# Kernel tuning notes

Hardware: AMD Instinct MI355X
Metric: run time of the kernel (lower is better)

## Reference

```python
import jax, jax.numpy as jnp
import numpy as np

N_NODES = 100000
HID = 128
N_LAYERS = 3
N_EDGES = 1600000
EPS = 1e-5


def setup_inputs() -> dict:
    key = jax.random.key(0)
    ks = jax.random.split(key, 10)
    H, L = HID, N_LAYERS
    # edge_index: row 0 = src, row 1 = dst (PyG source_to_target flow)
    edge_index = jax.random.randint(ks[0], (2, N_EDGES), 0, N_NODES, dtype=jnp.int32)
    # xavier-uniform embedding
    lim = float(np.sqrt(6.0 / (N_NODES + H)))
    emb = jax.random.uniform(ks[1], (N_NODES, H), jnp.float32, -lim, lim)
    s = 1.0 / np.sqrt(H)
    Wl = jax.random.uniform(ks[2], (L, H, H), jnp.float32, -s, s)  # lin_l (neighbors), has bias
    bl = jax.random.uniform(ks[3], (L, H), jnp.float32, -s, s)
    Wr = jax.random.uniform(ks[4], (L, H, H), jnp.float32, -s, s)  # lin_r (root), no bias
    ln_gamma = jnp.ones((L, H), jnp.float32)
    ln_beta = jnp.zeros((L, H), jnp.float32)
    sj = 1.0 / np.sqrt(H * (L + 1))
    jkW = jax.random.uniform(ks[5], (H, H * (L + 1)), jnp.float32, -sj, sj)
    jkb = jax.random.uniform(ks[6], (H,), jnp.float32, -sj, sj)
    return {"emb": emb, "Wl": Wl, "bl": bl, "Wr": Wr,
            "ln_gamma": ln_gamma, "ln_beta": ln_beta,
            "jkW": jkW, "jkb": jkb, "edge_index": edge_index}


def _layernorm(x, gamma, beta):
    mu = jnp.mean(x, axis=-1, keepdims=True)
    var = jnp.mean(jnp.square(x - mu), axis=-1, keepdims=True)
    return (x - mu) * jax.lax.rsqrt(var + EPS) * gamma + beta


def reference(emb, Wl, bl, Wr, ln_gamma, ln_beta, jkW, jkb, edge_index):
    src, dst = edge_index[0], edge_index[1]
    n = emb.shape[0]
    # in-degree for mean aggregation (clamped to avoid div-by-zero)
    deg = jax.ops.segment_sum(jnp.ones_like(dst, dtype=emb.dtype), dst, num_segments=n)
    inv_deg = (1.0 / jnp.maximum(deg, 1.0))[:, None]
    x = emb
    xs = [x]
    for i in range(N_LAYERS):
        x_prev = x
        # scatter-mean of neighbor features (gather [E,H] -> segment_sum [N,H])
        agg = jax.ops.segment_sum(x[src], dst, num_segments=n) * inv_deg
        # SAGEConv: lin_l(agg) + lin_r(x)
        x = agg @ Wl[i].T + bl[i] + x @ Wr[i].T
        x = _layernorm(x, ln_gamma[i], ln_beta[i])
        x = jax.nn.relu(x)
        # dropout is identity in eval mode
        if i > 0:
            x = x + x_prev
        xs.append(x)
    # jumping-knowledge concat + projection
    x = jnp.concatenate(xs, axis=1) @ jkW.T + jkb
    return x
```

## Files before the change

### kernel.cpp

```cpp
#include <hip/hip_runtime.h>
#include <hip/hip_bf16.h>
#include <stdint.h>

#define HID 128
#define BSHIFT 7
#define NBLK 64

typedef __attribute__((ext_vector_type(8))) __bf16 bf16x8;
typedef __attribute__((ext_vector_type(4))) float f32x4;

static __device__ __forceinline__ float bf2f(ushort h){
  union { uint u; float f; } c; c.u = ((uint)h) << 16; return c.f;
}
static __device__ __forceinline__ ushort f2bf(float f){
  union { float f; uint u; } c; c.f = f;
  uint u = c.u;
  return (ushort)((u + 0x7fffu + ((u >> 16) & 1u)) >> 16);
}
static __device__ __forceinline__ bf16x8 load8(const ushort* p){
  return *(const bf16x8*)p;
}

__global__ void k_cvt(const float* __restrict__ in, ushort* __restrict__ out, int n){
  int i = blockIdx.x * 256 + threadIdx.x;
  if (i < n) out[i] = f2bf(in[i]);
}

__global__ void k_cvtw(const float* __restrict__ Wl, const float* __restrict__ Wr,
                       ushort* __restrict__ outF, int total){
  int o = blockIdx.x * 256 + threadIdx.x;
  if (o >= total) return;
  int layer = o >> 15;
  int r = o & 32767;
  int e    = r & 7;
  int lane = (r >> 3) & 63;
  int jt   = (r >> 9) & 7;
  int mat  = (r >> 12) & 1;
  int kt   = r >> 13;
  int l16 = lane & 15, quad = lane >> 4;
  int j = l16 * 8 + jt;
  int k = kt * 32 + quad * 8 + e;
  const float* W = mat ? Wr : Wl;
  outF[o] = f2bf(W[layer * 16384 + j * 128 + k]);
}

__global__ void k_cvtjk(const float* __restrict__ jkW, ushort* __restrict__ outF){
  int o = blockIdx.x * 256 + threadIdx.x;
  int e    = o & 7;
  int lane = (o >> 3) & 63;
  int jt   = (o >> 9) & 7;
  int kt   = o >> 12;
  int l16 = lane & 15, quad = lane >> 4;
  int j = l16 * 4 + (jt & 3) + (jt >> 2) * 64;
  int k = kt * 32 + quad * 8 + e;
  outF[o] = f2bf(jkW[j * 512 + k]);
}

__global__ __launch_bounds__(1024) void k_count(
    const int* __restrict__ dst, int* __restrict__ rowcnt, int E, int NB, int es){
  __shared__ int h[1024];
  int blk = blockIdx.x;
  for (int i = threadIdx.x; i < NB; i += 1024) h[i] = 0;
  __syncthreads();
  int e0 = blk * es, e1 = min(e0 + es, E);
  for (int e = e0 + threadIdx.x; e < e1; e += 1024)
    atomicAdd(&h[dst[e] >> BSHIFT], 1);
  __syncthreads();
  for (int i = threadIdx.x; i < NB; i += 1024)
    rowcnt[blk * NB + i] = h[i];
}

__global__ __launch_bounds__(1024) void k_colscan(
    int* __restrict__ rowcnt, int* __restrict__ bbase, int NB, int nblk){
  int b = threadIdx.x;
  int total = 0;
  if (b < NB)
    for (int r = 0; r < nblk; r++) total += rowcnt[r * NB + b];
  int lane = b & 63, w = b >> 6;
  int x = total;
  #pragma unroll
  for (int d = 1; d < 64; d <<= 1){ int y = __shfl_up(x, d, 64); if (lane >= d) x += y; }
  __shared__ int tmp[16];
  if (lane == 63) tmp[w] = x;
  __syncthreads();
  if (b < 64){
    int s = (lane < 16) ? tmp[lane] : 0;
    #pragma unroll
    for (int d = 1; d < 16; d <<= 1){ int y = __shfl_up(s, d, 64); if (lane >= d) s += y; }
    if (lane < 16) tmp[lane] = s;
  }
  __syncthreads();
  int base = ((w > 0) ? tmp[w - 1] : 0) + x - total;
  if (b < NB){
    bbase[b] = base;
    int acc = base;
    for (int r = 0; r < nblk; r++){
      int v = rowcnt[r * NB + b];
      rowcnt[r * NB + b] = acc;
      acc += v;
    }
    if (b == NB - 1) bbase[NB] = acc;
  }
}

__global__ __launch_bounds__(1024) void k_place(
    const int* __restrict__ src, const int* __restrict__ dst,
    const int* __restrict__ rowcnt, uint* __restrict__ binned, int E, int NB, int es){
  __shared__ int cur[1024];
  int blk = blockIdx.x;
  for (int i = threadIdx.x; i < NB; i += 1024) cur[i] = rowcnt[blk * NB + i];
  __syncthreads();
  int e0 = blk * es, e1 = min(e0 + es, E);
  for (int e = e0 + threadIdx.x; e < e1; e += 1024){
    int d = dst[e];
    int b = d >> BSHIFT;
    int pos = atomicAdd(&cur[b], 1);
    binned[pos] = ((uint)src[e] << BSHIFT) | (uint)(d & 127);
  }
}

__global__ __launch_bounds__(256) void k_bpass(
    const uint* __restrict__ binned, const int* __restrict__ bbase,
    int* __restrict__ csr, int* __restrict__ offs, int* __restrict__ cnt, int N){
  int b = blockIdx.x;
  int n0 = b << BSHIFT;
  int tid = threadIdx.x;
  __shared__ int lcnt[128], loffs[128];
  if (tid < 128) lcnt[tid] = 0;
  __syncthreads();
  int base = bbase[b];
  int m = bbase[b + 1] - base;
  const uint* bp = binned + base;
  uint vv[12]; int slot[12];
  #pragma unroll
  for (int u = 0; u < 12; u++){
    int i = tid + u * 256;
    if (i < m){
      uint v = bp[i];
      vv[u] = v;
      slot[u] = atomicAdd(&lcnt[v & 127], 1);
    }
  }
  __syncthreads();
  if (tid < 64){
    int a0 = lcnt[tid * 2], a1 = lcnt[tid * 2 + 1];
    int s = a0 + a1;
    int x = s;
    #pragma unroll
    for (int d = 1; d < 64; d <<= 1){ int y = __shfl_up(x, d, 64); if (tid >= d) x += y; }
    int excl = x - s;
    loffs[tid * 2] = excl;
    loffs[tid * 2 + 1] = excl + a0;
  }
  __syncthreads();
  if (tid < 128 && n0 + tid < N){
    cnt[n0 + tid] = lcnt[tid];
    offs[n0 + tid] = base + loffs[tid];
  }
  #pragma unroll
  for (int u = 0; u < 12; u++){
    int i = tid + u * 256;
    if (i < m){
      uint v = vv[u];
      csr[base + loffs[v & 127] + slot[u]] = (int)(v >> BSHIFT);
    }
  }
}

__global__ __launch_bounds__(256) void k_aggregate(
    const ushort* __restrict__ x, const int* __restrict__ csr,
    const int* __restrict__ offs, const int* __restrict__ cnt,
    ushort* __restrict__ agg, int N){
  int node = blockIdx.x * 4 + (threadIdx.x >> 6);
  int lane = threadIdx.x & 63;
  if (node >= N) return;
  int half = lane >> 5;
  int l32  = lane & 31;
  int beg = offs[node], d = cnt[node];
  if (d == 0){
    if (half == 0){
      uint2 z = {0u, 0u};
      *(uint2*)(agg + (size_t)node * HID + l32 * 4) = z;
    }
    return;
  }
  const int* __restrict__ cp = csr + beg;
  float s0 = 0.f, s1 = 0.f, s2 = 0.f, s3 = 0.f;
  int i = 0;
  for (; i + 16 <= d; i += 16){
    int idx[8];
    #pragma unroll
    for (int u = 0; u < 8; u++) idx[u] = cp[i + 2 * u + half];
    uint2 v[8];
    #pragma unroll
    for (int u = 0; u < 8; u++)
      v[u] = *(const uint2*)(x + (size_t)idx[u] * HID + l32 * 4);
    #pragma unroll
    for (int u = 0; u < 8; u++){
      s0 += bf2f((ushort)v[u].x);
      s1 += bf2f((ushort)(v[u].x >> 16));
      s2 += bf2f((ushort)v[u].y);
      s3 += bf2f((ushort)(v[u].y >> 16));
    }
  }
  if (i < d){
    int idx[8]; float w[8];
    #pragma unroll
    for (int u = 0; u < 8; u++){
      int pos = i + 2 * u + half;
      bool ok = pos < d;
      pos = ok ? pos : d - 1;
      idx[u] = cp[pos];
      w[u] = ok ? 1.f : 0.f;
    }
    uint2 v[8];
    #pragma unroll
    for (int u = 0; u < 8; u++)
      v[u] = *(const uint2*)(x + (size_t)idx[u] * HID + l32 * 4);
    #pragma unroll
    for (int u = 0; u < 8; u++){
      s0 = fmaf(w[u], bf2f((ushort)v[u].x), s0);
      s1 = fmaf(w[u], bf2f((ushort)(v[u].x >> 16)), s1);
      s2 = fmaf(w[u], bf2f((ushort)v[u].y), s2);
      s3 = fmaf(w[u], bf2f((ushort)(v[u].y >> 16)), s3);
    }
  }
  s0 += __shfl_xor(s0, 32, 64);
  s1 += __shfl_xor(s1, 32, 64);
  s2 += __shfl_xor(s2, 32, 64);
  s3 += __shfl_xor(s3, 32, 64);
  if (half == 0){
    float inv = 1.0f / fmaxf((float)d, 1.0f);
    uint2 o;
    o.x = (uint)f2bf(s0 * inv) | ((uint)f2bf(s1 * inv) << 16);
    o.y = (uint)f2bf(s2 * inv) | ((uint)f2bf(s3 * inv) << 16);
    *(uint2*)(agg + (size_t)node * HID + l32 * 4) = o;
  }
}

template<int HAS_RES>
__global__ __launch_bounds__(256, 2) void k_layer(
    const ushort* __restrict__ agg, const ushort* __restrict__ xin,
    const ushort* __restrict__ Wf,
    const float* __restrict__ bl, const float* __restrict__ gamma,
    const float* __restrict__ beta,
    ushort* __restrict__ xout, int N, int nTiles){
  __shared__ ushort sB[32768];
  int tid = threadIdx.x;
  int wv = tid >> 6, lane = tid & 63;
  int quad = lane >> 4, l16 = lane & 15;

  #pragma unroll
  for (int i = 0; i < 16; i++){
    int c = i * 256 + tid;
    *(bf16x8*)(sB + c * 8) = load8(Wf + c * 8);
  }
  __syncthreads();

  float4 bi0 = *(const float4*)(bl + l16 * 8);
  float4 bi1 = *(const float4*)(bl + l16 * 8 + 4);
  float4 g0 = *(const float4*)(gamma + l16 * 8);
  float4 g1 = *(const float4*)(gamma + l16 * 8 + 4);
  float4 be0 = *(const float4*)(beta + l16 * 8);
  float4 be1 = *(const float4*)(beta + l16 * 8 + 4);
  float gg[8] = {g0.x, g0.y, g0.z, g0.w, g1.x, g1.y, g1.z, g1.w};
  float bb[8] = {be0.x, be0.y, be0.z, be0.w, be1.x, be1.y, be1.z, be1.w};
  float bia[8] = {bi0.x, bi0.y, bi0.z, bi0.w, bi1.x, bi1.y, bi1.z, bi1.w};

  for (int tile = blockIdx.x; tile < nTiles; tile += gridDim.x){
    int rowbase = tile * 128 + wv * 32;
    int r0 = rowbase + l16;      if (r0 >= N) r0 = N - 1;
    int r1 = rowbase + 16 + l16; if (r1 >= N) r1 = N - 1;

    bf16x8 aL0[4], aL1[4], aR0[4], aR1[4];
    #pragma unroll
    for (int kt = 0; kt < 4; kt++){
      int ao = kt * 32 + quad * 8;
      aL0[kt] = load8(agg + (size_t)r0 * HID + ao);
      aL1[kt] = load8(agg + (size_t)r1 * HID + ao);
      aR0[kt] = load8(xin + (size_t)r0 * HID + ao);
      aR1[kt] = load8(xin + (size_t)r1 * HID + ao);
    }

    f32x4 acc[2][8];
    #pragma unroll
    for (int jt = 0; jt < 8; jt++){
      float b = bia[jt];
      f32x4 c = {b, b, b, b};
      acc[0][jt] = c; acc[1][jt] = c;
    }

    #pragma unroll
    for (int kt = 0; kt < 4; kt++){
      #pragma unroll
      for (int jt = 0; jt < 8; jt++){
        bf16x8 bL = load8(sB + ((kt * 16 + jt) * 64 + lane) * 8);
        bf16x8 bR = load8(sB + ((kt * 16 + 8 + jt) * 64 + lane) * 8);
        acc[0][jt] = __builtin_amdgcn_mfma_f32_16x16x32_bf16(aL0[kt], bL, acc[0][jt], 0, 0, 0);
        acc[1][jt] = __builtin_amdgcn_mfma_f32_16x16x32_bf16(aL1[kt], bL, acc[1][jt], 0, 0, 0);
        acc[0][jt] = __builtin_amdgcn_mfma_f32_16x16x32_bf16(aR0[kt], bR, acc[0][jt], 0, 0, 0);
        acc[1][jt] = __builtin_amdgcn_mfma_f32_16x16x32_bf16(aR1[kt], bR, acc[1][jt], 0, 0, 0);
      }
    }

    #pragma unroll
    for (int rt = 0; rt < 2; rt++){
      float s1[4] = {0,0,0,0}, s2[4] = {0,0,0,0};
      #pragma unroll
      for (int jt = 0; jt < 8; jt++){
        #pragma unroll
        for (int r = 0; r < 4; r++){ float v = acc[rt][jt][r]; s1[r] += v; s2[r] += v * v; }
      }
      #pragma unroll
      for (int m = 1; m < 16; m <<= 1){
        #pragma unroll
        for (int r = 0; r < 4; r++){
          s1[r] += __shfl_xor(s1[r], m, 64);
          s2[r] += __shfl_xor(s2[r], m, 64);
        }
      }
      #pragma unroll
      for (int r = 0; r < 4; r++){
        float mu = s1[r] * (1.f / 128.f);
        float var = s2[r] * (1.f / 128.f) - mu * mu;
        float rs = rsqrtf(var + 1e-5f);
        int row = rowbase + rt * 16 + quad * 4 + r;
        int rowc = row < N ? row : N - 1;
        uint rw[4] = {0u, 0u, 0u, 0u};
        if (HAS_RES){
          uint4 rv = *(const uint4*)(xin + (size_t)rowc * HID + l16 * 8);
          rw[0] = rv.x; rw[1] = rv.y; rw[2] = rv.z; rw[3] = rv.w;
        }
        uint ow[4];
        #pragma unroll
        for (int p = 0; p < 4; p++){
          float v0 = (acc[rt][2 * p][r] - mu) * rs * gg[2 * p] + bb[2 * p];
          float v1 = (acc[rt][2 * p + 1][r] - mu) * rs * gg[2 * p + 1] + bb[2 * p + 1];
          v0 = fmaxf(v0, 0.f);
          v1 = fmaxf(v1, 0.f);
          if (HAS_RES){
            v0 += bf2f((ushort)(rw[p] & 0xffffu));
            v1 += bf2f((ushort)(rw[p] >> 16));
          }
          ow[p] = (uint)f2bf(v0) | ((uint)f2bf(v1) << 16);
        }
        uint4 o;
        o.x = ow[0]; o.y = ow[1]; o.z = ow[2]; o.w = ow[3];
        if (row < N)
          *(uint4*)(xout + (size_t)row * HID + l16 * 8) = o;
      }
    }
  }
}

__global__ __launch_bounds__(256, 2) void k_jk(
    const ushort* __restrict__ emb, const ushort* __restrict__ x1,
    const ushort* __restrict__ x2, const ushort* __restrict__ x3,
    const ushort* __restrict__ Wf,
    const float* __restrict__ jkb, float* __restrict__ out, int N, int nTiles){
  __shared__ ushort sB[32768];
  int tid = threadIdx.x;
  int wv = tid >> 6, lane = tid & 63;
  int quad = lane >> 4, l16 = lane & 15;

  float4 jb0 = *(const float4*)(jkb + l16 * 4);
  float4 jb1 = *(const float4*)(jkb + 64 + l16 * 4);
  float bia[8] = {jb0.x, jb0.y, jb0.z, jb0.w, jb1.x, jb1.y, jb1.z, jb1.w};

  for (int tile = blockIdx.x; tile < nTiles; tile += gridDim.x){
    int rowbase = tile * 128 + wv * 32;
    int r0 = rowbase + l16;      if (r0 >= N) r0 = N - 1;
    int r1 = rowbase + 16 + l16; if (r1 >= N) r1 = N - 1;

    f32x4 acc[2][8];
    #pragma unroll
    for (int jt = 0; jt < 8; jt++){
      float b = bia[jt];
      f32x4 c = {b, b, b, b};
      acc[0][jt] = c; acc[1][jt] = c;
    }

    #pragma unroll
    for (int h = 0; h < 2; h++){
      const ushort* sA = h ? x2 : emb;
      const ushort* sC = h ? x3 : x1;
      bf16x8 aA0[4], aA1[4], aC0[4], aC1[4];
      #pragma unroll
      for (int kt = 0; kt < 4; kt++){
        int ao = kt * 32 + quad * 8;
        aA0[kt] = load8(sA + (size_t)r0 * HID + ao);
        aA1[kt] = load8(sA + (size_t)r1 * HID + ao);
        aC0[kt] = load8(sC + (size_t)r0 * HID + ao);
        aC1[kt] = load8(sC + (size_t)r1 * HID + ao);
      }
      __syncthreads();
      const ushort* src = Wf + h * 32768;
      #pragma unroll
      for (int i = 0; i < 16; i++){
        int c = i * 256 + tid;
        *(bf16x8*)(sB + c * 8) = load8(src + c * 8);
      }
      __syncthreads();
      #pragma unroll
      for (int kt = 0; kt < 4; kt++){
        #pragma unroll
        for (int jt = 0; jt < 8; jt++){
          bf16x8 bA = load8(sB + ((kt * 8 + jt) * 64 + lane) * 8);
          bf16x8 bC = load8(sB + (((4 + kt) * 8 + jt) * 64 + lane) * 8);
          acc[0][jt] = __builtin_amdgcn_mfma_f32_16x16x32_bf16(aA0[kt], bA, acc[0][jt], 0, 0, 0);
          acc[1][jt] = __builtin_amdgcn_mfma_f32_16x16x32_bf16(aA1[kt], bA, acc[1][jt], 0, 0, 0);
          acc[0][jt] = __builtin_amdgcn_mfma_f32_16x16x32_bf16(aC0[kt], bC, acc[0][jt], 0, 0, 0);
          acc[1][jt] = __builtin_amdgcn_mfma_f32_16x16x32_bf16(aC1[kt], bC, acc[1][jt], 0, 0, 0);
        }
      }
    }

    #pragma unroll
    for (int rt = 0; rt < 2; rt++){
      #pragma unroll
      for (int r = 0; r < 4; r++){
        int row = rowbase + rt * 16 + quad * 4 + r;
        if (row < N){
          f32x4 v0 = {acc[rt][0][r], acc[rt][1][r], acc[rt][2][r], acc[rt][3][r]};
          f32x4 v1 = {acc[rt][4][r], acc[rt][5][r], acc[rt][6][r], acc[rt][7][r]};
          *(f32x4*)(out + (size_t)row * HID + l16 * 4) = v0;
          *(f32x4*)(out + (size_t)row * HID + 64 + l16 * 4) = v1;
        }
      }
    }
  }
}

extern "C" void kernel_launch(void* const* d_in, const int* in_sizes, int n_in,
                              void* d_out, int out_size, void* d_ws, size_t ws_size,
                              hipStream_t stream){
  const float* emb   = (const float*)d_in[0];
  const float* Wl    = (const float*)d_in[1];
  const float* bl    = (const float*)d_in[2];
  const float* Wr    = (const float*)d_in[3];
  const float* gamma = (const float*)d_in[4];
  const float* beta  = (const float*)d_in[5];
  const float* jkW   = (const float*)d_in[6];
  const float* jkb   = (const float*)d_in[7];
  const int*   eidx  = (const int*)d_in[8];
  int N = in_sizes[0] / HID;
  int E = in_sizes[8] / 2;
  const int* src = eidx;
  const int* dst = eidx + E;
  float* out = (float*)d_out;

  int NB = (N + 127) >> BSHIFT;
  int es = (E + NBLK - 1) / NBLK;

  char* w = (char*)d_ws;
  auto carve = [&](size_t bytes) -> char* {
    char* p = w; w += (bytes + 255) & ~(size_t)255; return p;
  };
  int Npad = ((N + 127) / 128) * 128;
  int* rowcnt   = (int*)carve((size_t)NBLK * NB * 4);
  int* bbase    = (int*)carve((size_t)(NB + 1) * 4);
  uint* binned  = (uint*)carve((size_t)E * 4);
  int* cnt      = (int*)carve((size_t)N * 4);
  int* offs     = (int*)carve((size_t)N * 4);
  int* csr      = (int*)carve((size_t)E * 4);
  ushort* Wfrag = (ushort*)carve((size_t)3 * 32768 * 2);
  ushort* jkWf  = (ushort*)carve((size_t)65536 * 2);
  ushort* embbf = (ushort*)carve((size_t)Npad * HID * 2);
  ushort* agg   = (ushort*)carve((size_t)Npad * HID * 2);
  ushort* x1    = (ushort*)carve((size_t)Npad * HID * 2);
  ushort* x2    = (ushort*)carve((size_t)Npad * HID * 2);
  ushort* x3    = (ushort*)carve((size_t)Npad * HID * 2);

  int nEmb = N * HID;
  k_cvtw<<<(3 * 32768 + 255) / 256, 256, 0, stream>>>(Wl, Wr, Wfrag, 3 * 32768);
  k_cvtjk<<<65536 / 256, 256, 0, stream>>>(jkW, jkWf);
  k_cvt<<<(nEmb + 255) / 256, 256, 0, stream>>>(emb, embbf, nEmb);

  k_count<<<NBLK, 1024, 0, stream>>>(dst, rowcnt, E, NB, es);
  k_colscan<<<1, 1024, 0, stream>>>(rowcnt, bbase, NB, NBLK);
  k_place<<<NBLK, 1024, 0, stream>>>(src, dst, rowcnt, binned, E, NB, es);
  k_bpass<<<NB, 256, 0, stream>>>(binned, bbase, csr, offs, cnt, N);

  int aggBlocks = (N + 3) / 4;
  int nTiles = (N + 127) / 128;
  int gemmGrid = nTiles < 512 ? nTiles : 512;

  k_aggregate<<<aggBlocks, 256, 0, stream>>>(embbf, csr, offs, cnt, agg, N);
  k_layer<0><<<gemmGrid, 256, 0, stream>>>(agg, embbf, Wfrag, bl, gamma, beta, x1, N, nTiles);
  k_aggregate<<<aggBlocks, 256, 0, stream>>>(x1, csr, offs, cnt, agg, N);
  k_layer<1><<<gemmGrid, 256, 0, stream>>>(agg, x1, Wfrag + 32768, bl + HID,
                                           gamma + HID, beta + HID, x2, N, nTiles);
  k_aggregate<<<aggBlocks, 256, 0, stream>>>(x2, csr, offs, cnt, agg, N);
  k_layer<1><<<gemmGrid, 256, 0, stream>>>(agg, x2, Wfrag + 2 * 32768, bl + 2 * HID,
                                           gamma + 2 * HID, beta + 2 * HID, x3, N, nTiles);
  k_jk<<<gemmGrid, 256, 0, stream>>>(embbf, x1, x2, x3, jkWf, jkb, out, N, nTiles);
}
```

Before: 631.4 us.

## Keep full JK weight resident in LDS and use 512-thread blocks in k_jk

The JK projection kernel now loads the whole bf16 jkW fragment (128 KB) into LDS once per block, instead of reloading two halves into LDS on every tile with two barriers each. Blocks become 512 threads covering 256-row tiles, and the grid is capped at 256. This removes the per-tile weight reload traffic and synchronisation. The cost is that 128 KB of LDS per block limits how many blocks fit on a CU, so occupancy is likely one block per CU despite the launch bound of 2.

Result: slower. 752.9 us (+19.2%).

```diff
diff --git a/kernel.cpp b/kernel.cpp
--- a/kernel.cpp
+++ b/kernel.cpp
@@ -353,22 +353,31 @@
   }
 }
 
-__global__ __launch_bounds__(256, 2) void k_jk(
+__global__ __launch_bounds__(512, 2) void k_jk(
     const ushort* __restrict__ emb, const ushort* __restrict__ x1,
     const ushort* __restrict__ x2, const ushort* __restrict__ x3,
     const ushort* __restrict__ Wf,
     const float* __restrict__ jkb, float* __restrict__ out, int N, int nTiles){
-  __shared__ ushort sB[32768];
+  __shared__ ushort sB[65536];
   int tid = threadIdx.x;
   int wv = tid >> 6, lane = tid & 63;
   int quad = lane >> 4, l16 = lane & 15;
 
+  #pragma unroll
+  for (int i = 0; i < 16; i++){
+    int c = i * 512 + tid;
+    *(bf16x8*)(sB + c * 8) = load8(Wf + c * 8);
+  }
+  __syncthreads();
+
   float4 jb0 = *(const float4*)(jkb + l16 * 4);
   float4 jb1 = *(const float4*)(jkb + 64 + l16 * 4);
   float bia[8] = {jb0.x, jb0.y, jb0.z, jb0.w, jb1.x, jb1.y, jb1.z, jb1.w};
 
+  const ushort* srcs[4] = {emb, x1, x2, x3};
+
   for (int tile = blockIdx.x; tile < nTiles; tile += gridDim.x){
-    int rowbase = tile * 128 + wv * 32;
+    int rowbase = tile * 256 + wv * 32;
     int r0 = rowbase + l16;      if (r0 >= N) r0 = N - 1;
     int r1 = rowbase + 16 + l16; if (r1 >= N) r1 = N - 1;
 
@@ -381,36 +390,23 @@
     }
 
     #pragma unroll
-    for (int h = 0; h < 2; h++){
-      const ushort* sA = h ? x2 : emb;
-      const ushort* sC = h ? x3 : x1;
-      bf16x8 aA0[4], aA1[4], aC0[4], aC1[4];
+    for (int s = 0; s < 4; s++){
+      const ushort* sp = srcs[s];
+      bf16x8 a0[4], a1[4];
       #pragma unroll
       for (int kt = 0; kt < 4; kt++){
         int ao = kt * 32 + quad * 8;
-        aA0[kt] = load8(sA + (size_t)r0 * HID + ao);
-        aA1[kt] = load8(sA + (size_t)r1 * HID + ao);
-        aC0[kt] = load8(sC + (size_t)r0 * HID + ao);
-        aC1[kt] = load8(sC + (size_t)r1 * HID + ao);
-      }
-      __syncthreads();
-      const ushort* src = Wf + h * 32768;
-      #pragma unroll
-      for (int i = 0; i < 16; i++){
-        int c = i * 256 + tid;
-        *(bf16x8*)(sB + c * 8) = load8(src + c * 8);
-      }
-      __syncthreads();
+        a0[kt] = load8(sp + (size_t)r0 * HID + ao);
+        a1[kt] = load8(sp + (size_t)r1 * HID + ao);
+      }
       #pragma unroll
       for (int kt = 0; kt < 4; kt++){
+        int ktg = s * 4 + kt;
         #pragma unroll
         for (int jt = 0; jt < 8; jt++){
-          bf16x8 bA = load8(sB + ((kt * 8 + jt) * 64 + lane) * 8);
-          bf16x8 bC = load8(sB + (((4 + kt) * 8 + jt) * 64 + lane) * 8);
-          acc[0][jt] = __builtin_amdgcn_mfma_f32_16x16x32_bf16(aA0[kt], bA, acc[0][jt], 0, 0, 0);
-          acc[1][jt] = __builtin_amdgcn_mfma_f32_16x16x32_bf16(aA1[kt], bA, acc[1][jt], 0, 0, 0);
-          acc[0][jt] = __builtin_amdgcn_mfma_f32_16x16x32_bf16(aC0[kt], bC, acc[0][jt], 0, 0, 0);
-          acc[1][jt] = __builtin_amdgcn_mfma_f32_16x16x32_bf16(aC1[kt], bC, acc[1][jt], 0, 0, 0);
+          bf16x8 bW = load8(sB + ((ktg * 8 + jt) * 64 + lane) * 8);
+          acc[0][jt] = __builtin_amdgcn_mfma_f32_16x16x32_bf16(a0[kt], bW, acc[0][jt], 0, 0, 0);
+          acc[1][jt] = __builtin_amdgcn_mfma_f32_16x16x32_bf16(a1[kt], bW, acc[1][jt], 0, 0, 0);
         }
       }
     }
@@ -456,7 +452,7 @@
   auto carve = [&](size_t bytes) -> char* {
     char* p = w; w += (bytes + 255) & ~(size_t)255; return p;
   };
-  int Npad = ((N + 127) / 128) * 128;
+  int Npad = ((N + 255) / 256) * 256;
   int* rowcnt   = (int*)carve((size_t)NBLK * NB * 4);
   int* bbase    = (int*)carve((size_t)(NB + 1) * 4);
   uint* binned  = (uint*)carve((size_t)E * 4);
@@ -484,6 +480,8 @@
   int aggBlocks = (N + 3) / 4;
   int nTiles = (N + 127) / 128;
   int gemmGrid = nTiles < 512 ? nTiles : 512;
+  int nTilesJK = (N + 255) / 256;
+  int jkGrid = nTilesJK < 256 ? nTilesJK : 256;
 
   k_aggregate<<<aggBlocks, 256, 0, stream>>>(embbf, csr, offs, cnt, agg, N);
   k_layer<0><<<gemmGrid, 256, 0, stream>>>(agg, embbf, Wfrag, bl, gamma, beta, x1, N, nTiles);
@@ -493,5 +491,5 @@
   k_aggregate<<<aggBlocks, 256, 0, stream>>>(x2, csr, offs, cnt, agg, N);
   k_layer<1><<<gemmGrid, 256, 0, stream>>>(agg, x2, Wfrag + 2 * 32768, bl + 2 * HID,
                                            gamma + 2 * HID, beta + 2 * HID, x3, N, nTiles);
-  k_jk<<<gemmGrid, 256, 0, stream>>>(embbf, x1, x2, x3, jkWf, jkb, out, N, nTiles);
-}
+  k_jk<<<jkGrid, 512, 0, stream>>>(embbf, x1, x2, x3, jkWf, jkb, out, N, nTilesJK);
+}
```
